# Performance work log

Measured on AMD Instinct MI355X. Metric: run time of the kernel, lower is better.

Reference implementation:

```python
import jax, jax.numpy as jnp
import numpy as np

B, T, D, H, NL = 8, 1024, 512, 8, 3
WS = (3, 5, 7)


def _mha(q_in, k_in, v_in, wq, bq, wk, bk, wv, bv, wo, bo):
    """Faithful copy of the torch MultiHeadAttention, including the
    transpose-free .view(B*H, -1, dh) head split (row-major reshape)."""
    bs = q_in.shape[0]
    dh = D // H
    q = (q_in @ wq + bq).reshape(bs * H, -1, dh)
    k = (k_in @ wk + bk).reshape(bs * H, -1, dh)
    v = (v_in @ wv + bv).reshape(bs * H, -1, dh)
    scores = jnp.einsum('bqd,bkd->bqk', q, k) / (dh ** 0.5)
    weights = jax.nn.softmax(scores, axis=-1)
    att = jnp.einsum('bqk,bkd->bqd', weights, v).reshape(bs, -1, D)
    return att @ wo + bo


def _forward(x, loc_wq, loc_bq, loc_wk, loc_bk, loc_wv, loc_bv, loc_wo, loc_bo,
             g_wq, g_bq, g_wk, g_bk, g_wv, g_bv, g_wo, g_bo, out_w, out_b):
    feats = []
    for lv in range(NL):
        w = WS[lv]
        pad = (w - 1) // 2
        xp = jnp.pad(x, ((0, 0), (pad, pad), (0, 0)))  # [B, T+2p, D]
        idx = jnp.arange(T)[:, None] + jnp.arange(w)[None, :]  # [T, w]
        win = xp[:, idx, :].reshape(B * T, w, D)  # sliding windows, same as unfold+permute
        lo = _mha(win, win, win,
                  loc_wq[lv], loc_bq[lv], loc_wk[lv], loc_bk[lv],
                  loc_wv[lv], loc_bv[lv], loc_wo[lv], loc_bo[lv])
        feats.append(lo.reshape(B, T, w, D).mean(axis=2))
    feats.append(_mha(x, x, x, g_wq, g_bq, g_wk, g_bk, g_wv, g_bv, g_wo, g_bo))
    combined = jnp.concatenate(feats, axis=-1)  # [B, T, D*(NL+1)]
    return combined @ out_w + out_b  # dropout is identity in eval mode


def setup_inputs() -> dict:
    key = jax.random.key(0)
    ks = jax.random.split(key, 20)
    s = 0.02
    d = {}
    d['x'] = jax.random.normal(ks[0], (B, T, D), jnp.float32)
    d['loc_wq'] = jax.random.normal(ks[1], (NL, D, D), jnp.float32) * s
    d['loc_bq'] = jax.random.normal(ks[2], (NL, D), jnp.float32) * s
    d['loc_wk'] = jax.random.normal(ks[3], (NL, D, D), jnp.float32) * s
    d['loc_bk'] = jax.random.normal(ks[4], (NL, D), jnp.float32) * s
    d['loc_wv'] = jax.random.normal(ks[5], (NL, D, D), jnp.float32) * s
    d['loc_bv'] = jax.random.normal(ks[6], (NL, D), jnp.float32) * s
    d['loc_wo'] = jax.random.normal(ks[7], (NL, D, D), jnp.float32) * s
    d['loc_bo'] = jax.random.normal(ks[8], (NL, D), jnp.float32) * s
    d['g_wq'] = jax.random.normal(ks[9], (D, D), jnp.float32) * s
    d['g_bq'] = jax.random.normal(ks[10], (D,), jnp.float32) * s
    d['g_wk'] = jax.random.normal(ks[11], (D, D), jnp.float32) * s
    d['g_bk'] = jax.random.normal(ks[12], (D,), jnp.float32) * s
    d['g_wv'] = jax.random.normal(ks[13], (D, D), jnp.float32) * s
    d['g_bv'] = jax.random.normal(ks[14], (D,), jnp.float32) * s
    d['g_wo'] = jax.random.normal(ks[15], (D, D), jnp.float32) * s
    d['g_bo'] = jax.random.normal(ks[16], (D,), jnp.float32) * s
    d['out_w'] = jax.random.normal(ks[17], (D * (NL + 1), D), jnp.float32) * s
    d['out_b'] = jax.random.normal(ks[18], (D,), jnp.float32) * s
    return d


def reference(x, loc_wq, loc_bq, loc_wk, loc_bk, loc_wv, loc_bv, loc_wo, loc_bo,
              g_wq, g_bq, g_wk, g_bk, g_wv, g_bv, g_wo, g_bo, out_w, out_b):
    return _forward(x, loc_wq, loc_bq, loc_wk, loc_bk, loc_wv, loc_bv, loc_wo, loc_bo,
                    g_wq, g_bq, g_wk, g_bk, g_wv, g_bv, g_wo, g_bo, out_w, out_b)
```

## Files before the change

### kernel.cpp

```cpp
#include <hip/hip_runtime.h>
#include <hip/hip_bf16.h>
#include <cstddef>

#define T_SEQ 1024
#define D_MODEL 512

typedef __attribute__((ext_vector_type(8))) __bf16 bf16x8;
typedef __attribute__((ext_vector_type(4))) float f32x4;
typedef __attribute__((ext_vector_type(16))) float f32x16;
typedef __attribute__((ext_vector_type(8))) unsigned short u16x8;
typedef __attribute__((ext_vector_type(4))) unsigned int u32x4;

typedef const unsigned int __attribute__((address_space(1)))* gas1_t;
typedef unsigned int __attribute__((address_space(3)))* las3_t;

__device__ __forceinline__ void gload_lds16(const void* g, void* l) {
  __builtin_amdgcn_global_load_lds((gas1_t)g, (las3_t)l, 16, 0, 0);
}

__device__ __forceinline__ float bf2f(unsigned short u) {
  return __uint_as_float(((unsigned)u) << 16);
}
__device__ __forceinline__ unsigned short f2bf(float f) {
  __hip_bfloat16 h = __float2bfloat16(f);
  return *(unsigned short*)&h;
}

#define CVTPK(dst, a, b) \
  asm("v_cvt_pk_bf16_f32 %0, %1, %2" : "=v"(dst) : "v"(a), "v"(b))

__device__ __forceinline__ void swap32(unsigned& a, unsigned& b, int lane) {
  const unsigned ax = __shfl_xor(a, 32);
  const unsigned bx = __shfl_xor(b, 32);
  const bool lo = lane < 32;
  const unsigned na = lo ? a : bx;
  const unsigned nb = lo ? ax : b;
  a = na; b = nb;
}

__global__ __launch_bounds__(256)
void prep_weights_kernel(const float* __restrict__ loc_wq, const float* __restrict__ loc_wk,
                         const float* __restrict__ loc_wv, const float* __restrict__ g_wq,
                         const float* __restrict__ g_wk, const float* __restrict__ g_wv,
                         const float* __restrict__ out_w, const float* __restrict__ loc_wo,
                         const float* __restrict__ g_wo, const float* __restrict__ x,
                         const float* __restrict__ loc_bq, const float* __restrict__ loc_bk,
                         const float* __restrict__ loc_bv,
                         __hip_bfloat16* __restrict__ WT, __hip_bfloat16* __restrict__ xb,
                         __hip_bfloat16* __restrict__ bqkvb) {
  __shared__ float tile[32][33];
  const size_t MS = (size_t)512 * 512;
  const int z = blockIdx.y;
  const int t = threadIdx.x;

  if (z == 20) {
    const int base = blockIdx.x * 16384 + t * 8;
#pragma unroll
    for (int it = 0; it < 8; ++it) {
      const int i = base + it * 2048;
      const float4 a = *(const float4*)(x + i);
      const float4 b = *(const float4*)(x + i + 4);
      u16x8 o;
      o[0] = f2bf(a.x); o[1] = f2bf(a.y); o[2] = f2bf(a.z); o[3] = f2bf(a.w);
      o[4] = f2bf(b.x); o[5] = f2bf(b.y); o[6] = f2bf(b.z); o[7] = f2bf(b.w);
      *(u16x8*)(xb + i) = o;
    }
    return;
  }
  if (z == 21) {
    const int i = blockIdx.x * 256 + t;
    if (blockIdx.x < 18) {
      const int which = i >> 9, lv = which / 3, role = which % 3, e = i & 511;
      const float* src = role == 0 ? loc_bq : role == 1 ? loc_bk : loc_bv;
      bqkvb[i] = __float2bfloat16(src[lv * 512 + e]);
    }
    return;
  }

  const float* src;
  bool tr = true;
  if (z < 3)       src = loc_wq + (size_t)z * MS;
  else if (z < 6)  src = loc_wk + (size_t)(z - 3) * MS;
  else if (z < 9)  src = loc_wv + (size_t)(z - 6) * MS;
  else if (z == 9)  src = g_wq;
  else if (z == 10) src = g_wk;
  else if (z == 11) src = g_wv;
  else if (z < 16) src = out_w + (size_t)(z - 12) * MS;
  else if (z < 19) { src = loc_wo + (size_t)(z - 16) * MS; tr = false; }
  else             { src = g_wo; tr = false; }
  __hip_bfloat16* dst = WT + (size_t)z * MS;

  const int tk = (blockIdx.x & 15) * 32;
  const int tn = (blockIdx.x >> 4) * 32;
  const int r = t >> 3, c4 = (t & 7) * 4;
  const float4 v = *(const float4*)(src + (size_t)(tk + r) * 512 + tn + c4);
  if (tr) {
    tile[r][c4 + 0] = v.x; tile[r][c4 + 1] = v.y;
    tile[r][c4 + 2] = v.z; tile[r][c4 + 3] = v.w;
    __syncthreads();
    ushort4 o;
    o.x = f2bf(tile[c4 + 0][r]); o.y = f2bf(tile[c4 + 1][r]);
    o.z = f2bf(tile[c4 + 2][r]); o.w = f2bf(tile[c4 + 3][r]);
    *(ushort4*)(dst + (size_t)(tn + r) * 512 + tk + c4) = o;
  } else {
    ushort4 o;
    o.x = f2bf(v.x); o.y = f2bf(v.y); o.z = f2bf(v.z); o.w = f2bf(v.w);
    *(ushort4*)(dst + (size_t)(tk + r) * 512 + tn + c4) = o;
  }
}

__device__ __forceinline__ void gemm_core_b128(
    const __hip_bfloat16* __restrict__ A, const __hip_bfloat16* __restrict__ BT,
    __hip_bfloat16* As, __hip_bfloat16* Bs, int row0, int col0, f32x4 acc[4][4]) {
  const int tid = threadIdx.x;
  const int wv = tid >> 6, lane = tid & 63;
  const int g = lane >> 4, r16 = lane & 15;
  const int wm = wv >> 1, wn = wv & 1;
  const char* Ab = (const char*)A;
  const char* Bb = (const char*)BT;
  for (int k0 = 0; k0 < 512; k0 += 32) {
    {
      const int row = tid >> 2, off = (tid & 3) << 4;
      gload_lds16(Ab + (size_t)(row0 + row) * 1024 + k0 * 2 + off,
                  (char*)As + (wv << 10));
      const int i2 = tid + 256;
      const int row2 = i2 >> 2, off2 = (i2 & 3) << 4;
      gload_lds16(Ab + (size_t)(row0 + row2) * 1024 + k0 * 2 + off2,
                  (char*)As + 4096 + (wv << 10));
    }
    {
      const int row = tid >> 2, off = (tid & 3) << 4;
      gload_lds16(Bb + (size_t)(col0 + row) * 1024 + k0 * 2 + off,
                  (char*)Bs + (wv << 10));
      const int i2 = tid + 256;
      const int row2 = i2 >> 2, off2 = (i2 & 3) << 4;
      gload_lds16(Bb + (size_t)(col0 + row2) * 1024 + k0 * 2 + off2,
                  (char*)Bs + 4096 + (wv << 10));
    }
    __syncthreads();
    bf16x8 a[4], b[4];
#pragma unroll
    for (int m = 0; m < 4; ++m)
      a[m] = *(const bf16x8*)(As + (wm * 64 + m * 16 + r16) * 32 + g * 8);
#pragma unroll
    for (int n = 0; n < 4; ++n)
      b[n] = *(const bf16x8*)(Bs + (wn * 64 + n * 16 + r16) * 32 + g * 8);
#pragma unroll
    for (int m = 0; m < 4; ++m)
#pragma unroll
      for (int n = 0; n < 4; ++n)
        acc[m][n] = __builtin_amdgcn_mfma_f32_16x16x32_bf16(a[m], b[n], acc[m][n], 0, 0, 0);
    __syncthreads();
  }
}

__device__ __forceinline__ void gemm_core_b64(
    const __hip_bfloat16* __restrict__ A, const __hip_bfloat16* __restrict__ BT,
    __hip_bfloat16* As, __hip_bfloat16* Bs, int row0, int col0, f32x4 acc[2][4]) {
  const int tid = threadIdx.x;
  const int wv = tid >> 6, lane = tid & 63;
  const int g = lane >> 4, r16 = lane & 15;
  const int wm = wv >> 1, wn = wv & 1;
  const char* Ab = (const char*)A;
  const char* Bb = (const char*)BT;
  for (int k0 = 0; k0 < 512; k0 += 32) {
    {
      const int row = tid >> 2, off = (tid & 3) << 4;
      gload_lds16(Ab + (size_t)(row0 + row) * 1024 + k0 * 2 + off,
                  (char*)As + (wv << 10));
    }
    {
      const int row = tid >> 2, off = (tid & 3) << 4;
      gload_lds16(Bb + (size_t)(col0 + row) * 1024 + k0 * 2 + off,
                  (char*)Bs + (wv << 10));
      const int i2 = tid + 256;
      const int row2 = i2 >> 2, off2 = (i2 & 3) << 4;
      gload_lds16(Bb + (size_t)(col0 + row2) * 1024 + k0 * 2 + off2,
                  (char*)Bs + 4096 + (wv << 10));
    }
    __syncthreads();
    bf16x8 a[2], b[4];
#pragma unroll
    for (int m = 0; m < 2; ++m)
      a[m] = *(const bf16x8*)(As + (wm * 32 + m * 16 + r16) * 32 + g * 8);
#pragma unroll
    for (int n = 0; n < 4; ++n)
      b[n] = *(const bf16x8*)(Bs + (wn * 64 + n * 16 + r16) * 32 + g * 8);
#pragma unroll
    for (int m = 0; m < 2; ++m)
#pragma unroll
      for (int n = 0; n < 4; ++n)
        acc[m][n] = __builtin_amdgcn_mfma_f32_16x16x32_bf16(a[m], b[n], acc[m][n], 0, 0, 0);
    __syncthreads();
  }
}

__device__ __forceinline__ void gemm_bias_body(
    const __hip_bfloat16* __restrict__ A, const __hip_bfloat16* __restrict__ WT,
    const float* __restrict__ bias, __hip_bfloat16* __restrict__ C,
    int row0, int col0, __hip_bfloat16* As, __hip_bfloat16* Bs) {
  f32x4 acc[4][4];
#pragma unroll
  for (int m = 0; m < 4; ++m)
#pragma unroll
    for (int n = 0; n < 4; ++n) acc[m][n] = (f32x4)(0.0f);
  gemm_core_b128(A, WT, As, Bs, row0, col0, acc);
  const int lane = threadIdx.x & 63, wv = threadIdx.x >> 6;
  const int g = lane >> 4, r16 = lane & 15, wm = wv >> 1, wn = wv & 1;
#pragma unroll
  for (int n = 0; n < 4; ++n) {
    const int col = col0 + wn * 64 + n * 16 + r16;
    const float bn = bias ? bias[col] : 0.f;
#pragma unroll
    for (int m = 0; m < 4; ++m) {
      const int rowb = row0 + wm * 64 + m * 16 + g * 4;
#pragma unroll
      for (int r = 0; r < 4; ++r)
        C[(size_t)(rowb + r) * 512 + col] = __float2bfloat16(acc[m][n][r] + bn);
    }
  }
}

__global__ __launch_bounds__(256)
void gemm_qkv_all_kernel(const __hip_bfloat16* __restrict__ A,
                         const __hip_bfloat16* __restrict__ WT_base,
                         const float* __restrict__ loc_bq, const float* __restrict__ loc_bk,
                         const float* __restrict__ loc_bv, const float* __restrict__ g_bq,
                         const float* __restrict__ g_bk, const float* __restrict__ g_bv,
                         __hip_bfloat16* __restrict__ proj_base) {
  __shared__ __attribute__((aligned(16))) __hip_bfloat16 As[4096];
  __shared__ __attribute__((aligned(16))) __hip_bfloat16 Bs[4096];
  const size_t MS = (size_t)512 * 512;
  const int z = blockIdx.z;
  const float* bias;
  if (z < 3)       bias = loc_bq + z * 512;
  else if (z < 6)  bias = loc_bk + (z - 3) * 512;
  else if (z < 9)  bias = loc_bv + (z - 6) * 512;
  else             bias = (z == 9) ? g_bq : (z == 10) ? g_bk : g_bv;
  gemm_bias_body(A, WT_base + (size_t)z * MS, bias,
                 proj_base + (size_t)z * (size_t)(8192 * 512),
                 blockIdx.y * 128, blockIdx.x * 128, As, Bs);
}

__global__ __launch_bounds__(256)
void gemm_qkv_kernel(const __hip_bfloat16* __restrict__ A,
                     const __hip_bfloat16* __restrict__ WT_base, size_t wt_stride,
                     const float* __restrict__ b0, const float* __restrict__ b1,
                     const float* __restrict__ b2,
                     __hip_bfloat16* __restrict__ out_base) {
  __shared__ __attribute__((aligned(16))) __hip_bfloat16 As[4096];
  __shared__ __attribute__((aligned(16))) __hip_bfloat16 Bs[4096];
  const int z = blockIdx.z;
  const float* bias = (z == 0) ? b0 : (z == 1) ? b1 : b2;
  gemm_bias_body(A, WT_base + (size_t)z * wt_stride, bias,
                 out_base + (size_t)z * (size_t)(8192 * 512),
                 blockIdx.y * 128, blockIdx.x * 128, As, Bs);
}

__global__ __launch_bounds__(256)
void gemm_fusew_kernel(const __hip_bfloat16* __restrict__ A_base,
                       const __hip_bfloat16* __restrict__ BT_base,
                       __hip_bfloat16* __restrict__ C_base) {
  __shared__ __attribute__((aligned(16))) __hip_bfloat16 As[4096];
  __shared__ __attribute__((aligned(16))) __hip_bfloat16 Bs[4096];
  const size_t MS = (size_t)512 * 512;
  const int z = blockIdx.z;
  f32x4 acc[4][4];
#pragma unroll
  for (int m = 0; m < 4; ++m)
#pragma unroll
    for (int n = 0; n < 4; ++n) acc[m][n] = (f32x4)(0.0f);
  gemm_core_b128(A_base + z * MS, BT_base + z * MS, As, Bs,
                 blockIdx.y * 128, blockIdx.x * 128, acc);
  __hip_bfloat16* C = C_base + z * MS;
  const int lane = threadIdx.x & 63, wv = threadIdx.x >> 6;
  const int g = lane >> 4, r16 = lane & 15, wm = wv >> 1, wn = wv & 1;
#pragma unroll
  for (int n = 0; n < 4; ++n) {
    const int col = blockIdx.x * 128 + wn * 64 + n * 16 + r16;
#pragma unroll
    for (int m = 0; m < 4; ++m) {
      const int rowb = blockIdx.y * 128 + wm * 64 + m * 16 + g * 4;
#pragma unroll
      for (int r = 0; r < 4; ++r)
        C[(size_t)(rowb + r) * 512 + col] = __float2bfloat16(acc[m][n][r]);
    }
  }
}

__global__ __launch_bounds__(256)
void bias_fuse_kernel(const float* __restrict__ loc_bo, const float* __restrict__ g_bo,
                      const float* __restrict__ out_w, const float* __restrict__ out_b,
                      float* __restrict__ bfused) {
  const int z = blockIdx.y;
  const int n = blockIdx.x * 256 + threadIdx.x;
  const float* bo = (z < 3) ? loc_bo + z * 512 : g_bo;
  const float* W = out_w + (size_t)z * 512 * 512;
  float acc = (z == 0) ? out_b[n] : 0.f;
  for (int m = 0; m < 512; ++m)
    acc = fmaf(bo[m], W[(size_t)m * 512 + n], acc);
  bfused[z * 512 + n] = acc;
}

template <int W>
__device__ __forceinline__ const __hip_bfloat16* slot_row(
    const __hip_bfloat16* __restrict__ X, const __hip_bfloat16* __restrict__ biasb,
    int b, int tloc, int pg, int sl, int* ch_out) {
  constexpr int PAD = (W - 1) / 2;
  const int hloc = sl >> 3, p = sl & 7;
  const int m = (pg * 4 + hloc) * W + p;
  const int j = m >> 3;
  *ch_out = m & 7;
  int sr = tloc + j - PAD;
  if (p < W) {
    if (sr >= 0 && sr < T_SEQ) return X + ((size_t)(b * T_SEQ + sr) << 9);
    return biasb;
  }
  sr = sr < 0 ? 0 : (sr > T_SEQ - 1 ? T_SEQ - 1 : sr);
  return X + ((size_t)(b * T_SEQ + sr) << 9);
}

template <int W>
__device__ __forceinline__ void local_attn_body(
    int bx, const __hip_bfloat16* __restrict__ Xq, const __hip_bfloat16* __restrict__ Xk,
    const __hip_bfloat16* __restrict__ Xv, const __hip_bfloat16* __restrict__ bqb,
    const __hip_bfloat16* __restrict__ bkb, const __hip_bfloat16* __restrict__ bvb,
    __hip_bfloat16* __restrict__ abar, unsigned* pool) {
  const int tid = threadIdx.x;
  const int wv = tid >> 6, lane = tid & 63;
  const int bt = bx * 4 + wv;
  const int b = bt >> 10, tloc = bt & 1023;
  unsigned* L = pool + wv * 2048;
  const int dl = lane & 31, hi = lane >> 5;

  {
    const int k2 = dl, dhalf = hi;
    int ch0, ch1;
    const __hip_bfloat16* r0 =
        slot_row<W>(Xv, bvb, b, tloc, (2 * k2) >> 5, (2 * k2) & 31, &ch0);
    const __hip_bfloat16* r1 =
        slot_row<W>(Xv, bvb, b, tloc, (2 * k2 + 1) >> 5, (2 * k2 + 1) & 31, &ch1);
    u16x8 A0[4], A1[4];
#pragma unroll
    for (int q = 0; q < 4; ++q) {
      A0[q] = *(const u16x8*)(r0 + ch0 * 64 + dhalf * 32 + q * 8);
      A1[q] = *(const u16x8*)(r1 + ch1 * 64 + dhalf * 32 + q * 8);
    }
#pragma unroll
    for (int q = 0; q < 4; ++q)
#pragma unroll
      for (int e = 0; e < 8; ++e) {
        const int d_ = dhalf * 32 + q * 8 + e;
        const unsigned dw = (unsigned)A0[q][e] | ((unsigned)A1[q][e] << 16);
        const int byte = (d_ * 128 + k2 * 4) ^ ((d_ & 7) << 4);
        L[byte >> 2] = dw;
      }
  }

  f32x16 accP[2][2];
#pragma unroll
  for (int pg = 0; pg < 2; ++pg)
#pragma unroll
    for (int dh = 0; dh < 2; ++dh) accP[pg][dh] = (f32x16)(0.0f);

  const int myb = dl >> 3;

#pragma unroll
  for (int pg = 0; pg < 2; ++pg) {
    int chK, chQ;
    const __hip_bfloat16* rK = slot_row<W>(Xk, bkb, b, tloc, pg, dl, &chK);
    const __hip_bfloat16* rQ = slot_row<W>(Xq, bqb, b, tloc, pg, dl, &chQ);
    f32x16 sa = (f32x16)(0.0f);
#pragma unroll
    for (int i = 0; i < 4; ++i) {
      const bf16x8 kf = *(const bf16x8*)(rK + chK * 64 + i * 16 + hi * 8);
      const bf16x8 qf = *(const bf16x8*)(rQ + chQ * 64 + i * 16 + hi * 8);
      sa = __builtin_amdgcn_mfma_f32_32x32x16_bf16(kf, qf, sa, 0, 0, 0);
    }

    float sel[4];
#pragma unroll
    for (int r4 = 0; r4 < 4; ++r4)
      sel[r4] = (myb == 0) ? sa[r4]
              : (myb == 1) ? sa[4 + r4]
              : (myb == 2) ? sa[8 + r4] : sa[12 + r4];

    float mx = -3e38f;
#pragma unroll
    for (int r4 = 0; r4 < 4; ++r4)
      if (r4 + 4 * hi < W) mx = fmaxf(mx, sel[r4]);
    mx = fmaxf(mx, __shfl_xor(mx, 32));
    float e[4], ls = 0.f;
#pragma unroll
    for (int r4 = 0; r4 < 4; ++r4) {
      e[r4] = (r4 + 4 * hi < W) ? __expf(0.125f * (sel[r4] - mx)) : 0.f;
      ls += e[r4];
    }
    ls += __shfl_xor(ls, 32);
    const float inv = 1.f / ls;

    unsigned dw0, dw1;
    CVTPK(dw0, e[0] * inv, e[1] * inv);
    CVTPK(dw1, e[2] * inv, e[3] * inv);
    const unsigned q0 = __shfl_xor(dw0, 32);
    const unsigned q1 = __shfl_xor(dw1, 32);

#pragma unroll
    for (int kh = 0; kh < 2; ++kh) {
      const bool on = (2 * kh + hi) == myb;
      u32x4 bw;
      if (hi == 0) { bw[0] = dw0; bw[1] = dw1; bw[2] = q0; bw[3] = q1; }
      else         { bw[0] = q0;  bw[1] = q1;  bw[2] = dw0; bw[3] = dw1; }
      if (!on) { bw[0] = 0u; bw[1] = 0u; bw[2] = 0u; bw[3] = 0u; }
      const bf16x8 pf = __builtin_bit_cast(bf16x8, bw);
#pragma unroll
      for (int dh = 0; dh < 2; ++dh) {
        const int d_ = dh * 32 + dl;
        const int off = (d_ * 128 + pg * 64 + kh * 32 + hi * 16) ^ ((d_ & 7) << 4);
        const bf16x8 va =
            __builtin_bit_cast(bf16x8, *(const u32x4*)((const char*)L + off));
        accP[pg][dh] = __builtin_amdgcn_mfma_f32_32x32x16_bf16(va, pf, accP[pg][dh], 0, 0, 0);
      }
    }
  }

#pragma unroll
  for (int pg = 0; pg < 2; ++pg) {
    if ((dl & 7) < W) {
      const int m_o = (pg * 4 + (dl >> 3)) * W + (dl & 7);
#pragma unroll
      for (int dh = 0; dh < 2; ++dh) {
#pragma unroll
        for (int rq = 0; rq < 4; ++rq) {
          unsigned wa, wb;
          CVTPK(wa, accP[pg][dh][4 * rq + 0], accP[pg][dh][4 * rq + 1]);
          CVTPK(wb, accP[pg][dh][4 * rq + 2], accP[pg][dh][4 * rq + 3]);
          const int dwi = m_o * 34 + dh * 16 + rq * 4 + hi * 2;
          uint2 w; w.x = wa; w.y = wb;
          *(uint2*)(L + dwi) = w;
        }
      }
    }
  }
  asm volatile("s_waitcnt lgkmcnt(0)" ::: "memory");

  const int cho = lane >> 3, fb = lane & 7;
  float o[8] = {0.f, 0.f, 0.f, 0.f, 0.f, 0.f, 0.f, 0.f};
#pragma unroll
  for (int jj = 0; jj < W; ++jj) {
    const int mo = 8 * jj + cho;
    const uint2 w0 = *(const uint2*)(L + mo * 34 + fb * 4);
    const uint2 w1 = *(const uint2*)(L + mo * 34 + fb * 4 + 2);
    o[0] += bf2f((unsigned short)(w0.x & 0xffff));
    o[1] += bf2f((unsigned short)(w0.x >> 16));
    o[2] += bf2f((unsigned short)(w0.y & 0xffff));
    o[3] += bf2f((unsigned short)(w0.y >> 16));
    o[4] += bf2f((unsigned short)(w1.x & 0xffff));
    o[5] += bf2f((unsigned short)(w1.x >> 16));
    o[6] += bf2f((unsigned short)(w1.y & 0xffff));
    o[7] += bf2f((unsigned short)(w1.y >> 16));
  }
  const float invw = 1.f / (float)W;
  u16x8 ov;
#pragma unroll
  for (int e2 = 0; e2 < 8; ++e2) ov[e2] = f2bf(o[e2] * invw);
  *(u16x8*)(abar + ((size_t)bt << 9) + cho * 64 + fb * 8) = ov;
}

template <int W>
__global__ __launch_bounds__(256)
void local_attn_mfma_kernel(const __hip_bfloat16* __restrict__ Xq,
                            const __hip_bfloat16* __restrict__ Xk,
                            const __hip_bfloat16* __restrict__ Xv,
                            const __hip_bfloat16* __restrict__ bqb,
                            const __hip_bfloat16* __restrict__ bkb,
                            const __hip_bfloat16* __restrict__ bvb,
                            __hip_bfloat16* __restrict__ abar) {
  __shared__ __attribute__((aligned(16))) unsigned pool[8192];
  const int bx = (blockIdx.x & 7) * 256 + (blockIdx.x >> 3);
  local_attn_body<W>(bx, Xq, Xk, Xv, bqb, bkb, bvb, abar, pool);
}

#define REDIST(pb, kb_)                                                  \
    {                                                                    \
      unsigned t0_, t1_, t2_, t3_, t4_, t5_, t6_, t7_;                   \
      CVTPK(t0_, pb[0], pb[1]);   CVTPK(t1_, pb[2], pb[3]);              \
      CVTPK(t2_, pb[4], pb[5]);   CVTPK(t3_, pb[6], pb[7]);              \
      CVTPK(t4_, pb[8], pb[9]);   CVTPK(t5_, pb[10], pb[11]);            \
      CVTPK(t6_, pb[12], pb[13]); CVTPK(t7_, pb[14], pb[15]);            \
      swap32(t0_, t2_, lane); swap32(t1_, t3_, lane);                    \
      swap32(t4_, t6_, lane); swap32(t5_, t7_, lane);                    \
      bw[kb_][0][0] = t0_; bw[kb_][0][1] = t1_; bw[kb_][0][2] = t2_;     \
      bw[kb_][0][3] = t3_;                                               \
      bw[kb_][1][0] = t4_; bw[kb_][1][1] = t5_; bw[kb_][1][2] = t6_;     \
      bw[kb_][1][3] = t7_;                                               \
    }

__device__ __forceinline__ void global_attn_body(
    int qblk, int bh, const __hip_bfloat16* __restrict__ Xq,
    const __hip_bfloat16* __restrict__ Xk, const __hip_bfloat16* __restrict__ Xv,
    __hip_bfloat16* __restrict__ att, unsigned* pool) {
  const int tid = threadIdx.x;
  const int lane = tid & 63;
  const int wv = tid >> 6;
  const size_t base = (size_t)bh << 16;
  const int c = lane & 31;
  const int g = lane >> 5;
  const int q0 = qblk * 128 + wv * 32;

  const __hip_bfloat16* Qp = Xq + base;
  const __hip_bfloat16* Kp = Xk + base;
  const __hip_bfloat16* Vp = Xv + base;

  bf16x8 qf[4];
#pragma unroll
  for (int s = 0; s < 4; ++s)
    qf[s] = *(const bf16x8*)(Qp + (size_t)(q0 + c) * 64 + s * 16 + g * 8);

  const int k2 = tid & 31, dblk = tid >> 5;

  bf16x8 kf[2][4];
  u16x8 v0, v1, v0n, v1n;

  v0 = *(const u16x8*)(Vp + (size_t)(2 * k2) * 64 + dblk * 8);
  v1 = *(const u16x8*)(Vp + (size_t)(2 * k2 + 1) * 64 + dblk * 8);
#pragma unroll
  for (int kb = 0; kb < 2; ++kb)
#pragma unroll
    for (int s = 0; s < 4; ++s)
      kf[kb][s] = *(const bf16x8*)(Kp + (size_t)(kb * 32 + c) * 64 + s * 16 + g * 8);

  f32x16 Oa = (f32x16)(0.0f), Ob = (f32x16)(0.0f);
  float m_run = -3e38f, l_run = 0.f;

  for (int kt = 0; kt < 16; ++kt) {
    unsigned* vb = pool + (kt & 1) * 2048;
#pragma unroll
    for (int jj = 0; jj < 8; ++jj) {
      const int d = dblk * 8 + jj;
      const unsigned dw = (unsigned)v0[jj] | ((unsigned)v1[jj] << 16);
      const int byte = (d * 128 + k2 * 4) ^ ((d & 7) << 4);
      vb[byte >> 2] = dw;
    }
    if (kt < 15) {
      const __hip_bfloat16* vsrc = Vp + (size_t)((kt + 1) * 64 + 2 * k2) * 64 + dblk * 8;
      v0n = *(const u16x8*)vsrc;
      v1n = *(const u16x8*)(vsrc + 64);
    }
    __syncthreads();

    f32x16 sa = (f32x16)(0.0f), sb = (f32x16)(0.0f);
#pragma unroll
    for (int s = 0; s < 4; ++s)
      sa = __builtin_amdgcn_mfma_f32_32x32x16_bf16(kf[0][s], qf[s], sa, 0, 0, 0);
#pragma unroll
    for (int s = 0; s < 4; ++s)
      sb = __builtin_amdgcn_mfma_f32_32x32x16_bf16(kf[1][s], qf[s], sb, 0, 0, 0);

    if (kt < 15) {
#pragma unroll
      for (int kb = 0; kb < 2; ++kb)
#pragma unroll
        for (int s = 0; s < 4; ++s)
          kf[kb][s] = *(const bf16x8*)(Kp + (size_t)((kt + 1) * 64 + kb * 32 + c) * 64 +
                                       s * 16 + g * 8);
    }

    float mx = sa[0];
#pragma unroll
    for (int r = 1; r < 16; ++r) mx = fmaxf(mx, sa[r]);
#pragma unroll
    for (int r = 0; r < 16; ++r) mx = fmaxf(mx, sb[r]);
    mx = fmaxf(mx, __shfl_xor(mx, 32));
    const float m_new = fmaxf(m_run, mx * 0.125f);
    const float alpha = __expf(m_run - m_new);

    float p0[16], p1[16];
    float lsum = 0.f;
#pragma unroll
    for (int r = 0; r < 16; ++r) { p0[r] = __expf(fmaf(sa[r], 0.125f, -m_new)); lsum += p0[r]; }
#pragma unroll
    for (int r = 0; r < 16; ++r) { p1[r] = __expf(fmaf(sb[r], 0.125f, -m_new)); lsum += p1[r]; }
    lsum += __shfl_xor(lsum, 32);
    l_run = fmaf(l_run, alpha, lsum);
    m_run = m_new;
#pragma unroll
    for (int r = 0; r < 16; ++r) { Oa[r] *= alpha; Ob[r] *= alpha; }

    unsigned bw[2][2][4];
    REDIST(p0, 0)
    REDIST(p1, 1)

    const unsigned* vbr = pool + (kt & 1) * 2048;
#pragma unroll
    for (int kb = 0; kb < 2; ++kb)
#pragma unroll
      for (int st = 0; st < 2; ++st) {
        const u32x4 pw = { bw[kb][st][0], bw[kb][st][1], bw[kb][st][2], bw[kb][st][3] };
        const bf16x8 pf = __builtin_bit_cast(bf16x8, pw);
        {
          const int row = c;
          const int off = (row * 128 + (kb * 64 + st * 32 + g * 16)) ^ ((row & 7) << 4);
          const bf16x8 va = __builtin_bit_cast(bf16x8, *(const u32x4*)((const char*)vbr + off));
          Oa = __builtin_amdgcn_mfma_f32_32x32x16_bf16(va, pf, Oa, 0, 0, 0);
        }
        {
          const int row = 32 + c;
          const int off = (row * 128 + (kb * 64 + st * 32 + g * 16)) ^ ((row & 7) << 4);
          const bf16x8 va = __builtin_bit_cast(bf16x8, *(const u32x4*)((const char*)vbr + off));
          Ob = __builtin_amdgcn_mfma_f32_32x32x16_bf16(va, pf, Ob, 0, 0, 0);
        }
      }

    v0 = v0n; v1 = v1n;
  }

  const float inv = 1.f / l_run;
  __hip_bfloat16* drow = att + base + (size_t)(q0 + c) * 64;
#pragma unroll
  for (int qd = 0; qd < 4; ++qd) {
    unsigned lo, hi2;
    {
      const float a0 = Oa[4 * qd + 0] * inv, a1 = Oa[4 * qd + 1] * inv;
      const float a2 = Oa[4 * qd + 2] * inv, a3 = Oa[4 * qd + 3] * inv;
      CVTPK(lo, a0, a1); CVTPK(hi2, a2, a3);
      uint2 w; w.x = lo; w.y = hi2;
      *(uint2*)(drow + 8 * qd + 4 * g) = w;
    }
    {
      const float a0 = Ob[4 * qd + 0] * inv, a1 = Ob[4 * qd + 1] * inv;
      const float a2 = Ob[4 * qd + 2] * inv, a3 = Ob[4 * qd + 3] * inv;
      CVTPK(lo, a0, a1); CVTPK(hi2, a2, a3);
      uint2 w; w.x = lo; w.y = hi2;
      *(uint2*)(drow + 32 + 8 * qd + 4 * g) = w;
    }
  }
}

__global__ __launch_bounds__(256)
void global_attn_mfma_kernel(const __hip_bfloat16* __restrict__ Xq,
                             const __hip_bfloat16* __restrict__ Xk,
                             const __hip_bfloat16* __restrict__ Xv,
                             __hip_bfloat16* __restrict__ att) {
  __shared__ __attribute__((aligned(16))) unsigned pool[4096];
  global_attn_body(blockIdx.y, blockIdx.x, Xq, Xk, Xv, att, pool);
}

__global__ __launch_bounds__(256)
void gemm_out_fused_kernel(const __hip_bfloat16* __restrict__ A0,
                           const __hip_bfloat16* __restrict__ A1,
                           const __hip_bfloat16* __restrict__ A2,
                           const __hip_bfloat16* __restrict__ A3,
                           const __hip_bfloat16* __restrict__ WT_base,
                           const float* __restrict__ bfused,
                           float* __restrict__ out) {
  __shared__ __attribute__((aligned(16))) __hip_bfloat16 As[2048];
  __shared__ __attribute__((aligned(16))) __hip_bfloat16 Bs[4096];
  const size_t MS = (size_t)512 * 512;
  const int row0 = blockIdx.y * 64, col0 = blockIdx.x * 128;
  f32x4 acc[2][4];
#pragma unroll
  for (int m = 0; m < 2; ++m)
#pragma unroll
    for (int n = 0; n < 4; ++n) acc[m][n] = (f32x4)(0.0f);
  const __hip_bfloat16* Az[4] = {A0, A1, A2, A3};
  for (int z = 0; z < 4; ++z)
    gemm_core_b64(Az[z], WT_base + (size_t)z * MS, As, Bs, row0, col0, acc);
  const int lane = threadIdx.x & 63, wv = threadIdx.x >> 6;
  const int g = lane >> 4, r16 = lane & 15, wm = wv >> 1, wn = wv & 1;
#pragma unroll
  for (int n = 0; n < 4; ++n) {
    const int col = col0 + wn * 64 + n * 16 + r16;
    const float bn = bfused[col] + bfused[512 + col] + bfused[1024 + col] +
                     bfused[1536 + col];
#pragma unroll
    for (int m = 0; m < 2; ++m) {
      const int rowb = row0 + wm * 32 + m * 16 + g * 4;
#pragma unroll
      for (int r = 0; r < 4; ++r)
        out[(size_t)(rowb + r) * 512 + col] = acc[m][n][r] + bn;
    }
  }
}

extern "C" void kernel_launch(void* const* d_in, const int* in_sizes, int n_in,
                              void* d_out, int out_size, void* d_ws, size_t ws_size,
                              hipStream_t stream) {
  const float* x      = (const float*)d_in[0];
  const float* loc_wq = (const float*)d_in[1];
  const float* loc_bq = (const float*)d_in[2];
  const float* loc_wk = (const float*)d_in[3];
  const float* loc_bk = (const float*)d_in[4];
  const float* loc_wv = (const float*)d_in[5];
  const float* loc_bv = (const float*)d_in[6];
  const float* loc_wo = (const float*)d_in[7];
  const float* loc_bo = (const float*)d_in[8];
  const float* g_wq  = (const float*)d_in[9];
  const float* g_bq  = (const float*)d_in[10];
  const float* g_wk  = (const float*)d_in[11];
  const float* g_bk  = (const float*)d_in[12];
  const float* g_wv  = (const float*)d_in[13];
  const float* g_bv  = (const float*)d_in[14];
  const float* g_wo  = (const float*)d_in[15];
  const float* g_bo  = (const float*)d_in[16];
  const float* out_w = (const float*)d_in[17];
  const float* out_b = (const float*)d_in[18];
  float* out = (float*)d_out;

  __hip_bfloat16* wsb = (__hip_bfloat16*)d_ws;
  const size_t SZ = (size_t)8192 * 512;
  const size_t MS = (size_t)512 * 512;

  __hip_bfloat16* xb    = wsb;
  __hip_bfloat16* WT    = wsb + SZ;
  float* bfused = (float*)(wsb + SZ + 24 * MS);
  __hip_bfloat16* bqkvb = wsb + SZ + 24 * MS + 4096;
  __hip_bfloat16* proj  = wsb + SZ + 24 * MS + 16384;

  const size_t need_big = 2 * (17 * SZ + 24 * MS + 16384);
  const bool big = ws_size >= need_big;

  const dim3 thr(256);

  prep_weights_kernel<<<dim3(256, 22), thr, 0, stream>>>(
      loc_wq, loc_wk, loc_wv, g_wq, g_wk, g_wv, out_w, loc_wo, g_wo,
      x, loc_bq, loc_bk, loc_bv, WT, xb, bqkvb);
  gemm_fusew_kernel<<<dim3(4, 4, 4), thr, 0, stream>>>(WT + 12 * MS, WT + 16 * MS,
                                                       WT + 20 * MS);
  bias_fuse_kernel<<<dim3(2, 4), thr, 0, stream>>>(loc_bo, g_bo, out_w, out_b, bfused);

  __hip_bfloat16 *abar0, *abar1, *abar2, *abar3;

  if (big) {
    abar0 = proj + 12 * SZ;
    abar1 = proj + 13 * SZ;
    abar2 = proj + 14 * SZ;
    abar3 = proj + 15 * SZ;
    gemm_qkv_all_kernel<<<dim3(4, 64, 12), thr, 0, stream>>>(
        xb, WT, loc_bq, loc_bk, loc_bv, g_bq, g_bk, g_bv, proj);
    local_attn_mfma_kernel<3><<<2048, thr, 0, stream>>>(
        proj + 0 * SZ, proj + 3 * SZ, proj + 6 * SZ,
        bqkvb + 0 * 512, bqkvb + 1 * 512, bqkvb + 2 * 512, abar0);
    local_attn_mfma_kernel<5><<<2048, thr, 0, stream>>>(
        proj + 1 * SZ, proj + 4 * SZ, proj + 7 * SZ,
        bqkvb + 3 * 512, bqkvb + 4 * 512, bqkvb + 5 * 512, abar1);
    local_attn_mfma_kernel<7><<<2048, thr, 0, stream>>>(
        proj + 2 * SZ, proj + 5 * SZ, proj + 8 * SZ,
        bqkvb + 6 * 512, bqkvb + 7 * 512, bqkvb + 8 * 512, abar2);
    global_attn_mfma_kernel<<<dim3(64, 8), thr, 0, stream>>>(
        proj + 9 * SZ, proj + 10 * SZ, proj + 11 * SZ, abar3);
  } else {
    __hip_bfloat16* Xq = proj;
    __hip_bfloat16* Xk = proj + SZ;
    __hip_bfloat16* Xv = proj + 2 * SZ;
    abar0 = proj + 3 * SZ;
    abar1 = proj + 4 * SZ;
    abar2 = proj + 5 * SZ;
    abar3 = proj + 6 * SZ;
    __hip_bfloat16* abars[3] = {abar0, abar1, abar2};
    const dim3 gqkv(4, 64, 3);
    for (int lv = 0; lv < 3; ++lv) {
      gemm_qkv_kernel<<<gqkv, thr, 0, stream>>>(
          xb, WT + lv * MS, 3 * MS,
          loc_bq + lv * 512, loc_bk + lv * 512, loc_bv + lv * 512, Xq);
      const __hip_bfloat16* bqb = bqkvb + (lv * 3 + 0) * 512;
      const __hip_bfloat16* bkb = bqkvb + (lv * 3 + 1) * 512;
      const __hip_bfloat16* bvb = bqkvb + (lv * 3 + 2) * 512;
      if (lv == 0)
        local_attn_mfma_kernel<3><<<2048, thr, 0, stream>>>(Xq, Xk, Xv, bqb, bkb, bvb, abars[lv]);
      else if (lv == 1)
        local_attn_mfma_kernel<5><<<2048, thr, 0, stream>>>(Xq, Xk, Xv, bqb, bkb, bvb, abars[lv]);
      else
        local_attn_mfma_kernel<7><<<2048, thr, 0, stream>>>(Xq, Xk, Xv, bqb, bkb, bvb, abars[lv]);
    }
    gemm_qkv_kernel<<<gqkv, thr, 0, stream>>>(xb, WT + 9 * MS, MS, g_bq, g_bk, g_bv, Xq);
    global_attn_mfma_kernel<<<dim3(64, 8), thr, 0, stream>>>(Xq, Xk, Xv, abar3);
  }

  gemm_out_fused_kernel<<<dim3(4, 128), thr, 0, stream>>>(abar0, abar1, abar2, abar3,
                                                          WT + 20 * MS, bfused, out);
}
```

Measured before the change: 288.2 us.

## Fold weight-fusion GEMM and bias fusion into QKV projection launch

Adds an extra z-slice to the QKV projection grid. Its blocks compute the Wo·out_w fused-weight GEMM tiles and the fused output bias that previously ran as two separate kernels, which removes two launches and lets that small work overlap with the projection GEMMs in the big-workspace path. The local attention kernel also gets a min-blocks-per-SM launch bound of 4, which may force register limits or spills. Most blocks in the extra slice exit immediately, and the fused-bias blocks run a serial 512-step loop that could lengthen the tail of the launch.

New measurement: 257.0 us (median of 2 runs). 10.8% less time.

```diff
diff --git a/kernel.cpp b/kernel.cpp
--- a/kernel.cpp
+++ b/kernel.cpp
@@ -221,17 +221,65 @@
   }
 }
 
+__device__ __forceinline__ void bias_fuse_body(
+    const float* __restrict__ bo, const float* __restrict__ W,
+    const float* __restrict__ add, float* __restrict__ bfz, int n) {
+  float acc = add ? add[n] : 0.f;
+  for (int m = 0; m < 512; ++m)
+    acc = fmaf(bo[m], W[(size_t)m * 512 + n], acc);
+  bfz[n] = acc;
+}
+
 __global__ __launch_bounds__(256)
 void gemm_qkv_all_kernel(const __hip_bfloat16* __restrict__ A,
                          const __hip_bfloat16* __restrict__ WT_base,
                          const float* __restrict__ loc_bq, const float* __restrict__ loc_bk,
                          const float* __restrict__ loc_bv, const float* __restrict__ g_bq,
                          const float* __restrict__ g_bk, const float* __restrict__ g_bv,
-                         __hip_bfloat16* __restrict__ proj_base) {
+                         const float* __restrict__ loc_bo, const float* __restrict__ g_bo,
+                         const float* __restrict__ out_w, const float* __restrict__ out_b,
+                         __hip_bfloat16* __restrict__ proj_base,
+                         float* __restrict__ bfused) {
   __shared__ __attribute__((aligned(16))) __hip_bfloat16 As[4096];
   __shared__ __attribute__((aligned(16))) __hip_bfloat16 Bs[4096];
   const size_t MS = (size_t)512 * 512;
   const int z = blockIdx.z;
+
+  if (z == 12) {
+    const int y = blockIdx.y;
+    if ((y & 12) == 0) {
+      const int wz = y >> 4, row = y & 3, col = blockIdx.x;
+      f32x4 acc[4][4];
+#pragma unroll
+      for (int m = 0; m < 4; ++m)
+#pragma unroll
+        for (int n = 0; n < 4; ++n) acc[m][n] = (f32x4)(0.0f);
+      gemm_core_b128(WT_base + (size_t)(12 + wz) * MS, WT_base + (size_t)(16 + wz) * MS,
+                     As, Bs, row * 128, col * 128, acc);
+      __hip_bfloat16* C = (__hip_bfloat16*)(WT_base + (size_t)(20 + wz) * MS);
+      const int lane = threadIdx.x & 63, wv = threadIdx.x >> 6;
+      const int g = lane >> 4, r16 = lane & 15, wm = wv >> 1, wn = wv & 1;
+#pragma unroll
+      for (int n = 0; n < 4; ++n) {
+        const int cc = col * 128 + wn * 64 + n * 16 + r16;
+#pragma unroll
+        for (int m = 0; m < 4; ++m) {
+          const int rowb = row * 128 + wm * 64 + m * 16 + g * 4;
+#pragma unroll
+          for (int r = 0; r < 4; ++r)
+            C[(size_t)(rowb + r) * 512 + cc] = __float2bfloat16(acc[m][n][r]);
+        }
+      }
+    } else if (((y & 15) == 4 || (y & 15) == 5) && blockIdx.x == 0) {
+      const int wz = y >> 4, half = y & 1;
+      const int n = half * 256 + threadIdx.x;
+      const float* bo = (wz < 3) ? loc_bo + wz * 512 : g_bo;
+      bias_fuse_body(bo, out_w + (size_t)wz * MS, wz == 0 ? out_b : nullptr,
+                     bfused + wz * 512, n);
+    }
+    return;
+  }
+
   const float* bias;
   if (z < 3)       bias = loc_bq + z * 512;
   else if (z < 6)  bias = loc_bk + (z - 3) * 512;
@@ -295,11 +343,8 @@
   const int z = blockIdx.y;
   const int n = blockIdx.x * 256 + threadIdx.x;
   const float* bo = (z < 3) ? loc_bo + z * 512 : g_bo;
-  const float* W = out_w + (size_t)z * 512 * 512;
-  float acc = (z == 0) ? out_b[n] : 0.f;
-  for (int m = 0; m < 512; ++m)
-    acc = fmaf(bo[m], W[(size_t)m * 512 + n], acc);
-  bfused[z * 512 + n] = acc;
+  bias_fuse_body(bo, out_w + (size_t)z * 512 * 512, z == 0 ? out_b : nullptr,
+                 bfused + z * 512, n);
 }
 
 template <int W>
@@ -468,7 +513,7 @@
 }
 
 template <int W>
-__global__ __launch_bounds__(256)
+__global__ __launch_bounds__(256, 4)
 void local_attn_mfma_kernel(const __hip_bfloat16* __restrict__ Xq,
                             const __hip_bfloat16* __restrict__ Xk,
                             const __hip_bfloat16* __restrict__ Xv,
@@ -725,9 +770,6 @@
   prep_weights_kernel<<<dim3(256, 22), thr, 0, stream>>>(
       loc_wq, loc_wk, loc_wv, g_wq, g_wk, g_wv, out_w, loc_wo, g_wo,
       x, loc_bq, loc_bk, loc_bv, WT, xb, bqkvb);
-  gemm_fusew_kernel<<<dim3(4, 4, 4), thr, 0, stream>>>(WT + 12 * MS, WT + 16 * MS,
-                                                       WT + 20 * MS);
-  bias_fuse_kernel<<<dim3(2, 4), thr, 0, stream>>>(loc_bo, g_bo, out_w, out_b, bfused);
 
   __hip_bfloat16 *abar0, *abar1, *abar2, *abar3;
 
@@ -736,8 +778,9 @@
     abar1 = proj + 13 * SZ;
     abar2 = proj + 14 * SZ;
     abar3 = proj + 15 * SZ;
-    gemm_qkv_all_kernel<<<dim3(4, 64, 12), thr, 0, stream>>>(
-        xb, WT, loc_bq, loc_bk, loc_bv, g_bq, g_bk, g_bv, proj);
+    gemm_qkv_all_kernel<<<dim3(4, 64, 13), thr, 0, stream>>>(
+        xb, WT, loc_bq, loc_bk, loc_bv, g_bq, g_bk, g_bv,
+        loc_bo, g_bo, out_w, out_b, proj, bfused);
     local_attn_mfma_kernel<3><<<2048, thr, 0, stream>>>(
         proj + 0 * SZ, proj + 3 * SZ, proj + 6 * SZ,
         bqkvb + 0 * 512, bqkvb + 1 * 512, bqkvb + 2 * 512, abar0);
@@ -750,6 +793,9 @@
     global_attn_mfma_kernel<<<dim3(64, 8), thr, 0, stream>>>(
         proj + 9 * SZ, proj + 10 * SZ, proj + 11 * SZ, abar3);
   } else {
+    gemm_fusew_kernel<<<dim3(4, 4, 4), thr, 0, stream>>>(WT + 12 * MS, WT + 16 * MS,
+                                                         WT + 20 * MS);
+    bias_fuse_kernel<<<dim3(2, 4), thr, 0, stream>>>(loc_bo, g_bo, out_w, out_b, bfused);
     __hip_bfloat16* Xq = proj;
     __hip_bfloat16* Xk = proj + SZ;
     __hip_bfloat16* Xv = proj + 2 * SZ;
```
